# Kernel tuning notes

Measured on AMD Instinct MI355X. Metric: run time of the kernel, lower is better.

The kernel has to match this reference:

```python
import jax, jax.numpy as jnp
import numpy as np

# static config (matches init_kwargs)
B, H, W, C = 8, 64, 64, 512
HEADS, WS, SHIFT = 16, 8, 4
N = WS * WS
HIDDEN = 4 * C
HEAD_DIM = C // HEADS
SCALE = HEAD_DIM ** -0.5
EPS = 1e-3  # keras LayerNormalization default epsilon


def _rel_pos_index(ws):
    # replicates tf.meshgrid default 'xy' indexing used in the source
    coords = np.stack(np.meshgrid(np.arange(ws), np.arange(ws)))  # [2, ws, ws]
    cf = coords.reshape(2, -1)
    rel = (cf[:, :, None] - cf[:, None, :]).transpose(1, 2, 0)  # [N, N, 2]
    rel[:, :, 0] += ws - 1
    rel[:, :, 1] += ws - 1
    rel[:, :, 0] *= 2 * ws - 1
    return jnp.asarray(rel.sum(-1))  # [N, N] int


def _attn_mask(h, w, ws, shift):
    img = np.zeros((h, w), dtype=np.float32)
    cnt = 0
    for hs in (slice(0, -ws), slice(-ws, -shift), slice(-shift, None)):
        for wsl in (slice(0, -ws), slice(-ws, -shift), slice(-shift, None)):
            img[hs, wsl] = cnt
            cnt += 1
    mw = img.reshape(h // ws, ws, w // ws, ws).transpose(0, 2, 1, 3).reshape(-1, ws * ws)  # [nW, N]
    diff = mw[:, None, :] - mw[:, :, None]
    return jnp.asarray(np.where(diff != 0, -100.0, 0.0).astype(np.float32))  # [nW, N, N]


REL_IDX = _rel_pos_index(WS)
ATTN_MASK = _attn_mask(H, W, WS, SHIFT)
NW = (H // WS) * (W // WS)


def _ln(x, g, b):
    mu = jnp.mean(x, -1, keepdims=True)
    var = jnp.mean(jnp.square(x - mu), -1, keepdims=True)
    return (x - mu) * jax.lax.rsqrt(var + EPS) * g + b


def setup_inputs() -> dict:
    key = jax.random.key(0)
    ks = jax.random.split(key, 14)
    s = 0.02
    return {
        "x": jax.random.normal(ks[0], (B, H * W, C), jnp.float32),
        "norm1_g": jnp.ones((C,), jnp.float32),
        "norm1_b": jnp.zeros((C,), jnp.float32),
        "qkv_w": jax.random.normal(ks[1], (C, 3 * C), jnp.float32) * s,
        "qkv_b": jnp.zeros((3 * C,), jnp.float32),
        "rpb_table": jax.random.normal(ks[2], ((2 * WS - 1) ** 2, HEADS), jnp.float32) * s,
        "proj_w": jax.random.normal(ks[3], (C, C), jnp.float32) * s,
        "proj_b": jnp.zeros((C,), jnp.float32),
        "norm2_g": jnp.ones((C,), jnp.float32),
        "norm2_b": jnp.zeros((C,), jnp.float32),
        "fc1_w": jax.random.normal(ks[4], (C, HIDDEN), jnp.float32) * s,
        "fc1_b": jnp.zeros((HIDDEN,), jnp.float32),
        "fc2_w": jax.random.normal(ks[5], (HIDDEN, C), jnp.float32) * s,
        "fc2_b": jnp.zeros((C,), jnp.float32),
    }


def reference(x, norm1_g, norm1_b, qkv_w, qkv_b, rpb_table, proj_w, proj_b,
              norm2_g, norm2_b, fc1_w, fc1_b, fc2_w, fc2_b):
    shortcut = x
    h = _ln(x, norm1_g, norm1_b).reshape(B, H, W, C)
    # cyclic shift (SW-MSA)
    h = jnp.roll(h, (-SHIFT, -SHIFT), axis=(1, 2))
    # window partition -> (B*nW, N, C)
    h = h.reshape(B, H // WS, WS, W // WS, WS, C).transpose(0, 1, 3, 2, 4, 5)
    h = h.reshape(B * NW, N, C)
    # qkv
    qkv = (h @ qkv_w + qkv_b).reshape(B * NW, N, 3, HEADS, HEAD_DIM).transpose(2, 0, 3, 1, 4)
    q, k, v = qkv[0] * SCALE, qkv[1], qkv[2]  # each [Bw, heads, N, hd]
    attn = jnp.einsum('bhnd,bhmd->bhnm', q, k)  # [Bw, heads, N, N]
    bias = rpb_table[REL_IDX.reshape(-1)].reshape(N, N, HEADS).transpose(2, 0, 1)
    attn = attn + bias[None]
    # shifted-window mask, per source: mask add -> softmax -> softmax AGAIN (source quirk)
    attn = attn.reshape(B, NW, HEADS, N, N) + ATTN_MASK[None, :, None]
    attn = attn.reshape(B * NW, HEADS, N, N)
    attn = jax.nn.softmax(attn, axis=-1)
    attn = jax.nn.softmax(attn, axis=-1)
    o = jnp.einsum('bhnm,bhmd->bhnd', attn, v).transpose(0, 2, 1, 3).reshape(B * NW, N, C)
    o = o @ proj_w + proj_b
    # window reverse + reverse shift
    o = o.reshape(B, H // WS, W // WS, WS, WS, C).transpose(0, 1, 3, 2, 4, 5).reshape(B, H, W, C)
    o = jnp.roll(o, (SHIFT, SHIFT), axis=(1, 2)).reshape(B, H * W, C)
    x = shortcut + o
    # MLP: source applies gelu twice (Dense activation + explicit gelu)
    y = _ln(x, norm2_g, norm2_b)
    y = jax.nn.gelu(jax.nn.gelu(y @ fc1_w + fc1_b, approximate=False), approximate=False)
    y = y @ fc2_w + fc2_b
    return x + y
```

## Files before the change

### kernel.cpp

```cpp
#include <hip/hip_runtime.h>
#include <hip/hip_bf16.h>
#include <math.h>


typedef unsigned short ushort_t;
typedef __attribute__((ext_vector_type(8))) short short8;
typedef __attribute__((ext_vector_type(8))) __bf16 bf16x8;
typedef __attribute__((ext_vector_type(4))) float f32x4;

#define DEVINL __device__ __forceinline__

union frag_u { short8 s; bf16x8 b; };

DEVINL float bf2f(ushort_t u){ union {unsigned int i; float f;} c; c.i = ((unsigned)u)<<16; return c.f; }
DEVINL ushort_t f2bf(float f){ union {unsigned int i; float f;} c; c.f = f; unsigned r = c.i + 0x7fffu + ((c.i>>16)&1u); return (ushort_t)(r>>16); }

typedef const __attribute__((address_space(1))) void* gas_t;
typedef __attribute__((address_space(3))) void* las_t;
DEVINL void load_lds16(const void* g, void* l) {
  __builtin_amdgcn_global_load_lds((gas_t)g, (las_t)l, 16, 0, 0);
}

DEVINL float gelu_fast(float v){
  float z  = fabsf(v) * 0.70710678118654752f;
  float t  = __builtin_amdgcn_rcpf(fmaf(0.47047f, z, 1.0f));
  float p  = t * fmaf(t, fmaf(t, 0.7478556f, -0.0958798f), 0.3480242f);
  float e  = __expf(-z*z);
  float er = fmaf(-p, e, 1.0f);
  float hs = (v >= 0.f) ? 0.5f : -0.5f;
  return v * fmaf(hs, er, 0.5f);
}

DEVINL int win_map_row(int t){
  int bw = t >> 6, n = t & 63;
  int b  = bw >> 6, wdx = bw & 63;
  int wh = wdx >> 3, ww = wdx & 7;
  int r  = n >> 3,  c  = n & 7;
  int hh = (wh*8 + r + 4) & 63;
  int w2 = (ww*8 + c + 4) & 63;
  return (b << 12) + (hh << 6) + w2;
}

DEVINL void remap_mn(int bid, int nwg, int nbn, int BM, int BN, int& m0, int& n0){
  int q    = nwg >> 3;
  int lbid = (bid & 7)*q + (bid >> 3);
  m0 = (lbid / nbn) * BM;
  n0 = (lbid % nbn) * BN;
}

__global__ void transpose_all(const float* __restrict__ qkv_w, const float* __restrict__ proj_w,
                              const float* __restrict__ fc1_w, const float* __restrict__ fc2_w,
                              ushort_t* __restrict__ wqT, ushort_t* __restrict__ wpT,
                              ushort_t* __restrict__ w1T, ushort_t* __restrict__ w2T){
  __shared__ float t[32][33];
  int bid = blockIdx.x;
  const float* in; ushort_t* out; int R, Ccols, bx, by;
  if (bid < 768)      { in=qkv_w;  out=wqT; R=512;  Ccols=1536; bx=(bid%48)*32;        by=(bid/48)*32; }
  else if (bid < 1024){ int b=bid-768;  in=proj_w; out=wpT; R=512;  Ccols=512;  bx=(b%16)*32; by=(b/16)*32; }
  else if (bid < 2048){ int b=bid-1024; in=fc1_w;  out=w1T; R=512;  Ccols=2048; bx=(b%64)*32; by=(b/64)*32; }
  else                { int b=bid-2048; in=fc2_w;  out=w2T; R=2048; Ccols=512;  bx=(b%16)*32; by=(b/16)*32; }
  int x = threadIdx.x, y = threadIdx.y;
  #pragma unroll
  for (int i=0;i<32;i+=8) t[y+i][x] = in[(size_t)(by+y+i)*Ccols + bx + x];
  __syncthreads();
  #pragma unroll
  for (int i=0;i<32;i+=8) out[(size_t)(bx+y+i)*R + by + x] = f2bf(t[x][y+i]);
}

__global__ __launch_bounds__(256) void ln_kernel(const float* __restrict__ in,
    const float* __restrict__ g, const float* __restrict__ bta,
    ushort_t* __restrict__ out, int windowed){
  int tid = threadIdx.x; int l = tid & 63; int w = tid >> 6;
  int t = blockIdx.x * 4 + w;
  int src = windowed ? win_map_row(t) : t;
  const float* row = in + (size_t)src * 512;
  float4 v0 = *(const float4*)(row + l*8);
  float4 v1 = *(const float4*)(row + l*8 + 4);
  float f[8] = {v0.x,v0.y,v0.z,v0.w, v1.x,v1.y,v1.z,v1.w};
  float s=0.f, s2=0.f;
  #pragma unroll
  for (int j=0;j<8;j++){ s += f[j]; s2 += f[j]*f[j]; }
  #pragma unroll
  for (int m=1;m<64;m<<=1){ s += __shfl_xor(s,m); s2 += __shfl_xor(s2,m); }
  float mu  = s * (1.f/512.f);
  float var = s2*(1.f/512.f) - mu*mu;
  float rs  = rsqrtf(var + 1e-3f);
  float4 g0 = *(const float4*)(g + l*8),   g1 = *(const float4*)(g + l*8 + 4);
  float4 b0 = *(const float4*)(bta + l*8), b1 = *(const float4*)(bta + l*8 + 4);
  float gg[8] = {g0.x,g0.y,g0.z,g0.w, g1.x,g1.y,g1.z,g1.w};
  float bb[8] = {b0.x,b0.y,b0.z,b0.w, b1.x,b1.y,b1.z,b1.w};
  short8 o;
  #pragma unroll
  for (int j=0;j<8;j++) o[j] = (short)f2bf((f[j]-mu)*rs*gg[j] + bb[j]);
  *(short8*)(out + (size_t)t*512 + l*8) = o;
}

#define G_STAGE(G, base, h, tt, LB) do { \
    load_lds16((G) + (base) + (size_t)((h)*128)*K    + (size_t)(tt)*64, &lds[(LB) + (h)*8192 +        w*512]); \
    load_lds16((G) + (base) + (size_t)((h)*128+64)*K + (size_t)(tt)*64, &lds[(LB) + (h)*8192 + 4096 + w*512]); \
  } while(0)

#define NOWAIT
#define VM4 asm volatile("s_waitcnt vmcnt(4)" ::: "memory")

#define PHASE(mp, STAGE_STMT, EXTRA) do { \
    bf16x8 a0 = *(const bf16x8*)&lds[ALb + aoff[2*(mp)  ][0]]; \
    bf16x8 a1 = *(const bf16x8*)&lds[ALb + aoff[2*(mp)  ][1]]; \
    bf16x8 a2 = *(const bf16x8*)&lds[ALb + aoff[2*(mp)+1][0]]; \
    bf16x8 a3 = *(const bf16x8*)&lds[ALb + aoff[2*(mp)+1][1]]; \
    STAGE_STMT; \
    EXTRA; \
    __builtin_amdgcn_s_barrier(); \
    asm volatile("s_waitcnt lgkmcnt(0)" ::: "memory"); \
    __builtin_amdgcn_sched_barrier(0); \
    __builtin_amdgcn_s_setprio(1); \
    _Pragma("unroll") \
    for (int nf=0; nf<4; nf++){ \
      acc[2*(mp)  ][nf] = __builtin_amdgcn_mfma_f32_16x16x32_bf16(a0, bfr[nf][0], acc[2*(mp)  ][nf], 0,0,0); \
      acc[2*(mp)  ][nf] = __builtin_amdgcn_mfma_f32_16x16x32_bf16(a1, bfr[nf][1], acc[2*(mp)  ][nf], 0,0,0); \
      acc[2*(mp)+1][nf] = __builtin_amdgcn_mfma_f32_16x16x32_bf16(a2, bfr[nf][0], acc[2*(mp)+1][nf], 0,0,0); \
      acc[2*(mp)+1][nf] = __builtin_amdgcn_mfma_f32_16x16x32_bf16(a3, bfr[nf][1], acc[2*(mp)+1][nf], 0,0,0); \
    } \
    __builtin_amdgcn_s_setprio(0); \
    __builtin_amdgcn_sched_barrier(0); \
    __builtin_amdgcn_s_barrier(); \
  } while(0)

template<int EPI>
__global__ __launch_bounds__(512, 2) void gemm256(
    const ushort_t* __restrict__ A, const ushort_t* __restrict__ Bt,
    const float* __restrict__ bias, void* __restrict__ Cout_v,
    const float* __restrict__ xres, int M, int N, int K, int nbn)
{
  __shared__ ushort_t lds[65536];
  const int tid = threadIdx.x; const int l = tid & 63; const int w = tid >> 6;
  const int wm = w >> 2, wn = w & 3;
  int m0, n0;
  remap_mn(blockIdx.x, gridDim.x, nbn, 256, 256, m0, n0);
  const int lr = l & 15, lk = l >> 4;
  const int nt = K >> 6;

  const int r0 = tid >> 3;
  const int kc = ((tid & 7) - r0) & 7;
  const size_t aRow0 = (size_t)(m0 + r0) * K + kc * 8;
  const size_t bRow0 = (size_t)(n0 + r0) * K + kc * 8;

  int aoff[8][2], boff[4][2];
  #pragma unroll
  for (int mf=0; mf<8; mf++){
    int row = wm*128 + mf*16 + lr;
    #pragma unroll
    for (int kh=0; kh<2; kh++){ int c = kh*4 + lk; aoff[mf][kh] = (row*8 + ((c + row)&7))*8; }
  }
  #pragma unroll
  for (int nf=0; nf<4; nf++){
    int row = wn*64 + nf*16 + lr;
    #pragma unroll
    for (int kh=0; kh<2; kh++){ int c = kh*4 + lk; boff[nf][kh] = (row*8 + ((c + row)&7))*8; }
  }

  f32x4 acc[8][4] = {};

  G_STAGE(A,  aRow0, 0, 0, 0);
  G_STAGE(A,  aRow0, 1, 0, 0);
  G_STAGE(Bt, bRow0, 0, 0, 16384);
  G_STAGE(Bt, bRow0, 1, 0, 16384);
  G_STAGE(Bt, bRow0, 0, 1, 32768+16384);
  G_STAGE(Bt, bRow0, 1, 1, 32768+16384);
  VM4;
  __builtin_amdgcn_s_barrier();

  for (int t = 0; t < nt; ++t) {
    const int b   = t & 1;
    const int ALb = b*32768, BLb = ALb + 16384;
    const int ALn = (b^1)*32768;
    const int t1  = (t+1 < nt) ? t+1 : t;
    const int t2  = (t+2 < nt) ? t+2 : t;

    bf16x8 bfr[4][2];
    #pragma unroll
    for (int nf=0; nf<4; nf++){
      bfr[nf][0] = *(const bf16x8*)&lds[BLb + boff[nf][0]];
      bfr[nf][1] = *(const bf16x8*)&lds[BLb + boff[nf][1]];
    }
    PHASE(0, G_STAGE(A,  aRow0, 0, t1, ALn), NOWAIT);
    PHASE(1, G_STAGE(A,  aRow0, 1, t1, ALn), NOWAIT);
    PHASE(2, G_STAGE(Bt, bRow0, 0, t2, BLb), NOWAIT);
    PHASE(3, G_STAGE(Bt, bRow0, 1, t2, BLb), VM4);
  }

  asm volatile("s_waitcnt vmcnt(0)" ::: "memory");
  __builtin_amdgcn_s_barrier();

  int erow = l >> 2, ecc = l & 3;
  if (EPI == 0){
    ushort_t* tw = lds + w*1152;
    #pragma unroll
    for (int mf=0; mf<8; mf++){
      #pragma unroll
      for (int nf=0; nf<4; nf++){
        float bz = bias[n0 + wn*64 + nf*16 + lr];
        #pragma unroll
        for (int rg=0; rg<4; rg++)
          tw[(lk*4+rg)*72 + nf*16 + lr] = f2bf(acc[mf][nf][rg] + bz);
      }
      short8 p0 = *(const short8*)(tw + erow*72 + ecc*16);
      short8 p1 = *(const short8*)(tw + erow*72 + ecc*16 + 8);
      int grow = m0 + wm*128 + mf*16 + erow;
      int col  = n0 + wn*64 + ecc*16;
      *(short8*)&((ushort_t*)Cout_v)[(size_t)grow*N + col]     = p0;
      *(short8*)&((ushort_t*)Cout_v)[(size_t)grow*N + col + 8] = p1;
    }
  } else {
    float* twf = (float*)lds + w*1152;
    #pragma unroll
    for (int mf=0; mf<8; mf++){
      #pragma unroll
      for (int nf=0; nf<4; nf++){
        float bz = bias[n0 + wn*64 + nf*16 + lr];
        #pragma unroll
        for (int rg=0; rg<4; rg++)
          twf[(lk*4+rg)*72 + nf*16 + lr] = acc[mf][nf][rg] + bz;
      }
      int grow = m0 + wm*128 + mf*16 + erow;
      int col  = n0 + wn*64 + ecc*16;
      float4 q0 = *(const float4*)(twf + erow*72 + ecc*16);
      float4 q1 = *(const float4*)(twf + erow*72 + ecc*16 + 4);
      float4 q2 = *(const float4*)(twf + erow*72 + ecc*16 + 8);
      float4 q3 = *(const float4*)(twf + erow*72 + ecc*16 + 12);
      size_t off;
      if (EPI == 2){
        int row2 = win_map_row(grow);
        off = (size_t)row2*512 + col;
        float4 x0 = *(const float4*)(xres + off);
        float4 x1 = *(const float4*)(xres + off + 4);
        float4 x2 = *(const float4*)(xres + off + 8);
        float4 x3 = *(const float4*)(xres + off + 12);
        q0 = make_float4(q0.x+x0.x, q0.y+x0.y, q0.z+x0.z, q0.w+x0.w);
        q1 = make_float4(q1.x+x1.x, q1.y+x1.y, q1.z+x1.z, q1.w+x1.w);
        q2 = make_float4(q2.x+x2.x, q2.y+x2.y, q2.z+x2.z, q2.w+x2.w);
        q3 = make_float4(q3.x+x3.x, q3.y+x3.y, q3.z+x3.z, q3.w+x3.w);
      } else {
        off = (size_t)grow*N + col;
        float* o = (float*)Cout_v;
        float4 x0 = *(const float4*)(o + off);
        float4 x1 = *(const float4*)(o + off + 4);
        float4 x2 = *(const float4*)(o + off + 8);
        float4 x3 = *(const float4*)(o + off + 12);
        q0 = make_float4(q0.x+x0.x, q0.y+x0.y, q0.z+x0.z, q0.w+x0.w);
        q1 = make_float4(q1.x+x1.x, q1.y+x1.y, q1.z+x1.z, q1.w+x1.w);
        q2 = make_float4(q2.x+x2.x, q2.y+x2.y, q2.z+x2.z, q2.w+x2.w);
        q3 = make_float4(q3.x+x3.x, q3.y+x3.y, q3.z+x3.z, q3.w+x3.w);
      }
      float* o = (float*)Cout_v;
      *(float4*)(o + off)      = q0;
      *(float4*)(o + off + 4)  = q1;
      *(float4*)(o + off + 8)  = q2;
      *(float4*)(o + off + 12) = q3;
    }
  }
}

template<int EPI>
__global__ __launch_bounds__(512, 4) void gemmv(
    const ushort_t* __restrict__ A, const ushort_t* __restrict__ Bt,
    const float* __restrict__ bias, void* __restrict__ Cout_v,
    const float* __restrict__ xres, int M, int N, int K, int nbn)
{
  __shared__ ushort_t lds[24576];
  __shared__ float g2tab[(EPI==1)?2048:1];
  const int tid = threadIdx.x; const int l = tid & 63; const int w = tid >> 6;
  const int wm = w >> 1, wn = w & 1;
  int m0, n0; remap_mn(blockIdx.x, gridDim.x, nbn, 256, 128, m0, n0);
  const int lr = l & 15, lk = l >> 4;
  const int nt = K >> 5;

  if (EPI == 1){
    #pragma unroll
    for (int i=0;i<4;i++){
      int idx = tid*4 + i;
      float vi = -4.f + (float)idx*(1.f/256.f);
      g2tab[idx] = gelu_fast(gelu_fast(vi));
    }
  }

  const int r0 = tid >> 2;
  const int kc = ((tid & 3) - (r0 >> 1)) & 3;
  const size_t aG = (size_t)(m0 + r0) * K + kc*8;
  const size_t bG = (size_t)(n0 + r0) * K + kc*8;

  #define STAGE_T(tt, LB) do { \
    load_lds16(A  + aG +                  (size_t)(tt)*32, &lds[(LB) +        w*512]); \
    load_lds16(A  + aG + 128*(size_t)K +  (size_t)(tt)*32, &lds[(LB) + 4096 + w*512]); \
    load_lds16(Bt + bG +                  (size_t)(tt)*32, &lds[(LB) + 8192 + w*512]); \
  } while(0)

  int aoff[4], boff[4];
  #pragma unroll
  for (int mf=0; mf<4; mf++){
    int row = wm*64 + mf*16 + lr;
    aoff[mf] = (row*4 + ((lk + (row>>1)) & 3))*8;
  }
  #pragma unroll
  for (int nf=0; nf<4; nf++){
    int row = wn*64 + nf*16 + lr;
    boff[nf] = 8192 + (row*4 + ((lk + (row>>1)) & 3))*8;
  }

  f32x4 acc[4][4] = {};

  STAGE_T(0, 0);
  STAGE_T(1, 12288);
  asm volatile("s_waitcnt vmcnt(3)" ::: "memory");
  __builtin_amdgcn_s_barrier();

  for (int t = 0; t < nt; ++t){
    const int Lb = (t & 1) ? 12288 : 0;
    const int t2 = (t+2 < nt) ? t+2 : nt-1;
    bf16x8 af[4], bfr[4];
    #pragma unroll
    for (int mf=0; mf<4; mf++) af[mf]  = *(const bf16x8*)&lds[Lb + aoff[mf]];
    #pragma unroll
    for (int nf=0; nf<4; nf++) bfr[nf] = *(const bf16x8*)&lds[Lb + boff[nf]];
    __builtin_amdgcn_sched_barrier(0);
    asm volatile("s_waitcnt lgkmcnt(0)" ::: "memory");
    __builtin_amdgcn_s_barrier();
    __builtin_amdgcn_sched_barrier(0);
    STAGE_T(t2, Lb);
    __builtin_amdgcn_sched_barrier(0);
    __builtin_amdgcn_s_setprio(1);
    #pragma unroll
    for (int mf=0; mf<4; mf++)
      #pragma unroll
      for (int nf=0; nf<4; nf++)
        acc[mf][nf] = __builtin_amdgcn_mfma_f32_16x16x32_bf16(af[mf], bfr[nf], acc[mf][nf], 0,0,0);
    __builtin_amdgcn_s_setprio(0);
    __builtin_amdgcn_sched_barrier(0);
    asm volatile("s_waitcnt vmcnt(3)" ::: "memory");
    __builtin_amdgcn_s_barrier();
  }

  asm volatile("s_waitcnt vmcnt(0)" ::: "memory");
  __builtin_amdgcn_s_barrier();
  __builtin_amdgcn_sched_barrier(0);

  int erow = l >> 2, ecc = l & 3;
  ushort_t* tw = lds + w*1152;
  #pragma unroll
  for (int mf=0; mf<4; mf++){
    #pragma unroll
    for (int nf=0; nf<4; nf++){
      float bz = bias[n0 + wn*64 + nf*16 + lr];
      #pragma unroll
      for (int rg=0; rg<4; rg++){
        float v = acc[mf][nf][rg] + bz;
        if (EPI == 1){
          float u  = fminf(fmaxf(fmaf(v, 256.f, 1024.5f), 0.f), 2047.f);
          float rr = g2tab[(int)u];
          rr = (v >  4.f) ? v   : rr;
          v  = (v < -4.f) ? 0.f : rr;
        }
        tw[(lk*4+rg)*72 + nf*16 + lr] = f2bf(v);
      }
    }
    short8 p0 = *(const short8*)(tw + erow*72 + ecc*16);
    short8 p1 = *(const short8*)(tw + erow*72 + ecc*16 + 8);
    int grow = m0 + wm*64 + mf*16 + erow;
    int col  = n0 + wn*64 + ecc*16;
    *(short8*)&((ushort_t*)Cout_v)[(size_t)grow*N + col]     = p0;
    *(short8*)&((ushort_t*)Cout_v)[(size_t)grow*N + col + 8] = p1;
  }
  #undef STAGE_T
}

DEVINL int band3(int t){ return (t<56) ? 0 : ((t<60) ? 1 : 2); }

__global__ __launch_bounds__(256) void attn_kernel(const ushort_t* __restrict__ qkv,
    const float* __restrict__ rpb, ushort_t* __restrict__ o)
{
  __shared__ ushort_t sP[4][64*64];
  __shared__ ushort_t sV[4][64*32];
  int tid = threadIdx.x; int l = tid & 63; int w = tid >> 6;
  int p = blockIdx.x*4 + w;
  int bw = p >> 4, head = p & 15;
  int lr = l & 15, lk = l >> 4;
  const ushort_t* base = qkv + (size_t)bw*64*1536 + head*32;

  #pragma unroll
  for (int c=0;c<4;c++){
    int idx = c*64 + l;
    int row = idx >> 2, cc = idx & 3;
    load_lds16(base + 1024 + (size_t)row*1536 + cc*8, &sV[w][0] + c*512);
  }

  bf16x8 qf[4], kf[4];
  #pragma unroll
  for (int m=0;m<4;m++) qf[m] = *(const bf16x8*)(base +       (size_t)(m*16+lr)*1536 + lk*8);
  #pragma unroll
  for (int m=0;m<4;m++) kf[m] = *(const bf16x8*)(base + 512 + (size_t)(m*16+lr)*1536 + lk*8);

  f32x4 s[4][4] = {};
  #pragma unroll
  for (int m=0;m<4;m++)
    #pragma unroll
    for (int n=0;n<4;n++)
      s[m][n] = __builtin_amdgcn_mfma_f32_16x16x32_bf16(qf[m], kf[n], s[m][n], 0,0,0);

  int wdx = bw & 63; int wh = wdx >> 3, ww = wdx & 7;
  const float SCALE = 0.17677669529663687f;
  #pragma unroll
  for (int m=0;m<4;m++){
    #pragma unroll
    for (int r=0;r<4;r++){
      int i  = m*16 + lk*4 + r;
      int ri = band3(wh*8 + (i>>3))*3 + band3(ww*8 + (i&7));
      int ix = i & 7, iy = i >> 3;
      #pragma unroll
      for (int n=0;n<4;n++){
        int j   = n*16 + lr;
        int rj  = band3(wh*8 + (j>>3))*3 + band3(ww*8 + (j&7));
        int idx = 15*(ix - (j&7) + 7) + (iy - (j>>3) + 7);
        float bv = rpb[idx*16 + head];
        float mk = (ri == rj) ? 0.f : -100.f;
        s[m][n][r] = s[m][n][r]*SCALE + bv + mk;
      }
    }
  }

  #pragma unroll
  for (int pass=0; pass<2; pass++){
    #pragma unroll
    for (int m=0;m<4;m++){
      #pragma unroll
      for (int r=0;r<4;r++){
        float mx = fmaxf(fmaxf(s[m][0][r], s[m][1][r]), fmaxf(s[m][2][r], s[m][3][r]));
        #pragma unroll
        for (int d=1;d<16;d<<=1) mx = fmaxf(mx, __shfl_xor(mx, d));
        float sum = 0.f;
        #pragma unroll
        for (int n=0;n<4;n++){ float e = __expf(s[m][n][r]-mx); s[m][n][r]=e; sum += e; }
        #pragma unroll
        for (int d=1;d<16;d<<=1) sum += __shfl_xor(sum, d);
        float inv = 1.f/sum;
        #pragma unroll
        for (int n=0;n<4;n++) s[m][n][r] = s[m][n][r]*inv;
      }
    }
  }

  ushort_t* pl = &sP[w][0];
  #pragma unroll
  for (int m=0;m<4;m++)
    #pragma unroll
    for (int r=0;r<4;r++){
      int i = m*16 + lk*4 + r;
      #pragma unroll
      for (int n=0;n<4;n++){
        int j = n*16 + lr;
        int byte = i*128 + ((j*2) ^ ((i&7)<<4));
        pl[byte>>1] = f2bf(s[m][n][r]);
      }
    }

  asm volatile("s_waitcnt vmcnt(0)" ::: "memory");
  const ushort_t* vl = &sV[w][0];
  frag_u vf[2][2];
  #pragma unroll
  for (int kb=0;kb<2;kb++)
    #pragma unroll
    for (int nb=0;nb<2;nb++){
      #pragma unroll
      for (int j=0;j<8;j++){
        int k = kb*32 + lk*8 + j;
        vf[kb][nb].s[j] = (short)vl[k*32 + nb*16 + lr];
      }
    }

  f32x4 oacc[4][2] = {};
  #pragma unroll
  for (int m=0;m<4;m++){
    #pragma unroll
    for (int kb=0;kb<2;kb++){
      int row  = m*16 + lr;
      int byte = row*128 + ((kb*64 + lk*16) ^ ((row&7)<<4));
      bf16x8 pf = *(const bf16x8*)(pl + (byte>>1));
      #pragma unroll
      for (int nb=0;nb<2;nb++)
        oacc[m][nb] = __builtin_amdgcn_mfma_f32_16x16x32_bf16(pf, vf[kb][nb].b, oacc[m][nb], 0,0,0);
    }
  }

  ushort_t* orow = o + (size_t)bw*64*512 + head*32;
  #pragma unroll
  for (int m=0;m<4;m++)
    #pragma unroll
    for (int nb=0;nb<2;nb++)
      #pragma unroll
      for (int r=0;r<4;r++){
        int i = m*16 + lk*4 + r;
        int d = nb*16 + lr;
        orow[(size_t)i*512 + d] = f2bf(oacc[m][nb][r]);
      }
}

extern "C" void kernel_launch(void* const* d_in, const int* in_sizes, int n_in,
                              void* d_out, int out_size, void* d_ws, size_t ws_size,
                              hipStream_t stream) {
  const float* x      = (const float*)d_in[0];
  const float* n1g    = (const float*)d_in[1];
  const float* n1b    = (const float*)d_in[2];
  const float* qkv_w  = (const float*)d_in[3];
  const float* qkv_b  = (const float*)d_in[4];
  const float* rpb    = (const float*)d_in[5];
  const float* proj_w = (const float*)d_in[6];
  const float* proj_b = (const float*)d_in[7];
  const float* n2g    = (const float*)d_in[8];
  const float* n2b    = (const float*)d_in[9];
  const float* fc1_w  = (const float*)d_in[10];
  const float* fc1_b  = (const float*)d_in[11];
  const float* fc2_w  = (const float*)d_in[12];
  const float* fc2_b  = (const float*)d_in[13];
  float* out = (float*)d_out;

  ushort_t* ws = (ushort_t*)d_ws;
  size_t off = 0;
  ushort_t* wqT = ws + off; off += (size_t)1536*512;
  ushort_t* wpT = ws + off; off += (size_t)512*512;
  ushort_t* w1T = ws + off; off += (size_t)2048*512;
  ushort_t* w2T = ws + off; off += (size_t)512*2048;
  ushort_t* R1  = ws + off; off += (size_t)32768*512;
  ushort_t* R2  = ws + off; off += (size_t)32768*2048;
  if (ws_size < off*sizeof(ushort_t)) return;

  transpose_all<<<3072, dim3(32,8), 0, stream>>>(qkv_w, proj_w, fc1_w, fc2_w, wqT, wpT, w1T, w2T);

  ln_kernel<<<8192, 256, 0, stream>>>(x, n1g, n1b, R1, 1);
  gemm256<0><<<768, 512, 0, stream>>>(R1, wqT, qkv_b, R2, nullptr, 32768, 1536, 512, 6);
  attn_kernel<<<2048, 256, 0, stream>>>(R2, rpb, R1);
  gemm256<2><<<256, 512, 0, stream>>>(R1, wpT, proj_b, out, x, 32768, 512, 512, 2);
  ln_kernel<<<8192, 256, 0, stream>>>(out, n2g, n2b, R1, 0);
  gemmv<1><<<2048, 512, 0, stream>>>(R1, w1T, fc1_b, R2, nullptr, 32768, 2048, 512, 16);
  gemm256<3><<<256, 512, 0, stream>>>(R2, w2T, fc2_b, out, nullptr, 32768, 512, 2048, 2);
}
```

Before: 389.5 us.

## Triple-buffer gemm K loop and route fc2 through smaller-tile kernel

The 256x128 tiled GEMM grows from double to triple LDS buffering, prefetching three K-steps ahead so more global loads are in flight. To fit the larger LDS footprint, the GELU lookup table is halved to 1024 entries at coarser resolution. A new fp32 accumulate-into-output epilogue lets the fc2 GEMM use this kernel, giving 512 blocks instead of 256 with the larger 256x256 kernel and so better occupancy across CUs. The trade-offs are more LDS per block, which may reduce resident blocks, and a coarser GELU approximation.

```diff
diff --git a/kernel.cpp b/kernel.cpp
--- a/kernel.cpp
+++ b/kernel.cpp
@@ -229,6 +229,7 @@
       float4 q2 = *(const float4*)(twf + erow*72 + ecc*16 + 8);
       float4 q3 = *(const float4*)(twf + erow*72 + ecc*16 + 12);
       size_t off;
+      float* o = (float*)Cout_v;
       if (EPI == 2){
         int row2 = win_map_row(grow);
         off = (size_t)row2*512 + col;
@@ -242,7 +243,6 @@
         q3 = make_float4(q3.x+x3.x, q3.y+x3.y, q3.z+x3.z, q3.w+x3.w);
       } else {
         off = (size_t)grow*N + col;
-        float* o = (float*)Cout_v;
         float4 x0 = *(const float4*)(o + off);
         float4 x1 = *(const float4*)(o + off + 4);
         float4 x2 = *(const float4*)(o + off + 8);
@@ -252,7 +252,6 @@
         q2 = make_float4(q2.x+x2.x, q2.y+x2.y, q2.z+x2.z, q2.w+x2.w);
         q3 = make_float4(q3.x+x3.x, q3.y+x3.y, q3.z+x3.z, q3.w+x3.w);
       }
-      float* o = (float*)Cout_v;
       *(float4*)(o + off)      = q0;
       *(float4*)(o + off + 4)  = q1;
       *(float4*)(o + off + 8)  = q2;
@@ -262,13 +261,13 @@
 }
 
 template<int EPI>
-__global__ __launch_bounds__(512, 4) void gemmv(
+__global__ __launch_bounds__(512, 4) void gemmw(
     const ushort_t* __restrict__ A, const ushort_t* __restrict__ Bt,
     const float* __restrict__ bias, void* __restrict__ Cout_v,
     const float* __restrict__ xres, int M, int N, int K, int nbn)
 {
-  __shared__ ushort_t lds[24576];
-  __shared__ float g2tab[(EPI==1)?2048:1];
+  __shared__ ushort_t lds[36864];
+  __shared__ float g2tab[(EPI==1)?1024:1];
   const int tid = threadIdx.x; const int l = tid & 63; const int w = tid >> 6;
   const int wm = w >> 1, wn = w & 1;
   int m0, n0; remap_mn(blockIdx.x, gridDim.x, nbn, 256, 128, m0, n0);
@@ -277,9 +276,9 @@
 
   if (EPI == 1){
     #pragma unroll
-    for (int i=0;i<4;i++){
-      int idx = tid*4 + i;
-      float vi = -4.f + (float)idx*(1.f/256.f);
+    for (int i=0;i<2;i++){
+      int idx = tid*2 + i;
+      float vi = -4.f + (float)idx*(1.f/128.f);
       g2tab[idx] = gelu_fast(gelu_fast(vi));
     }
   }
@@ -311,12 +310,13 @@
 
   STAGE_T(0, 0);
   STAGE_T(1, 12288);
-  asm volatile("s_waitcnt vmcnt(3)" ::: "memory");
+  STAGE_T(2, 24576);
+  asm volatile("s_waitcnt vmcnt(6)" ::: "memory");
   __builtin_amdgcn_s_barrier();
 
+  int Lb = 0;
   for (int t = 0; t < nt; ++t){
-    const int Lb = (t & 1) ? 12288 : 0;
-    const int t2 = (t+2 < nt) ? t+2 : nt-1;
+    const int t3 = (t+3 < nt) ? t+3 : nt-1;
     bf16x8 af[4], bfr[4];
     #pragma unroll
     for (int mf=0; mf<4; mf++) af[mf]  = *(const bf16x8*)&lds[Lb + aoff[mf]];
@@ -326,7 +326,7 @@
     asm volatile("s_waitcnt lgkmcnt(0)" ::: "memory");
     __builtin_amdgcn_s_barrier();
     __builtin_amdgcn_sched_barrier(0);
-    STAGE_T(t2, Lb);
+    STAGE_T(t3, Lb);
     __builtin_amdgcn_sched_barrier(0);
     __builtin_amdgcn_s_setprio(1);
     #pragma unroll
@@ -336,8 +336,9 @@
         acc[mf][nf] = __builtin_amdgcn_mfma_f32_16x16x32_bf16(af[mf], bfr[nf], acc[mf][nf], 0,0,0);
     __builtin_amdgcn_s_setprio(0);
     __builtin_amdgcn_sched_barrier(0);
-    asm volatile("s_waitcnt vmcnt(3)" ::: "memory");
+    asm volatile("s_waitcnt vmcnt(6)" ::: "memory");
     __builtin_amdgcn_s_barrier();
+    Lb += 12288; if (Lb == 36864) Lb = 0;
   }
 
   asm volatile("s_waitcnt vmcnt(0)" ::: "memory");
@@ -345,30 +346,62 @@
   __builtin_amdgcn_sched_barrier(0);
 
   int erow = l >> 2, ecc = l & 3;
-  ushort_t* tw = lds + w*1152;
-  #pragma unroll
-  for (int mf=0; mf<4; mf++){
-    #pragma unroll
-    for (int nf=0; nf<4; nf++){
-      float bz = bias[n0 + wn*64 + nf*16 + lr];
-      #pragma unroll
-      for (int rg=0; rg<4; rg++){
-        float v = acc[mf][nf][rg] + bz;
-        if (EPI == 1){
-          float u  = fminf(fmaxf(fmaf(v, 256.f, 1024.5f), 0.f), 2047.f);
+  if (EPI == 1){
+    ushort_t* tw = lds + w*1152;
+    #pragma unroll
+    for (int mf=0; mf<4; mf++){
+      #pragma unroll
+      for (int nf=0; nf<4; nf++){
+        float bz = bias[n0 + wn*64 + nf*16 + lr];
+        #pragma unroll
+        for (int rg=0; rg<4; rg++){
+          float v = acc[mf][nf][rg] + bz;
+          float u  = fminf(fmaxf(fmaf(v, 128.f, 512.5f), 0.f), 1023.f);
           float rr = g2tab[(int)u];
           rr = (v >  4.f) ? v   : rr;
           v  = (v < -4.f) ? 0.f : rr;
+          tw[(lk*4+rg)*72 + nf*16 + lr] = f2bf(v);
         }
-        tw[(lk*4+rg)*72 + nf*16 + lr] = f2bf(v);
-      }
-    }
-    short8 p0 = *(const short8*)(tw + erow*72 + ecc*16);
-    short8 p1 = *(const short8*)(tw + erow*72 + ecc*16 + 8);
-    int grow = m0 + wm*64 + mf*16 + erow;
-    int col  = n0 + wn*64 + ecc*16;
-    *(short8*)&((ushort_t*)Cout_v)[(size_t)grow*N + col]     = p0;
-    *(short8*)&((ushort_t*)Cout_v)[(size_t)grow*N + col + 8] = p1;
+      }
+      short8 p0 = *(const short8*)(tw + erow*72 + ecc*16);
+      short8 p1 = *(const short8*)(tw + erow*72 + ecc*16 + 8);
+      int grow = m0 + wm*64 + mf*16 + erow;
+      int col  = n0 + wn*64 + ecc*16;
+      *(short8*)&((ushort_t*)Cout_v)[(size_t)grow*N + col]     = p0;
+      *(short8*)&((ushort_t*)Cout_v)[(size_t)grow*N + col + 8] = p1;
+    }
+  } else {
+    float* twf = (float*)lds + w*1152;
+    #pragma unroll
+    for (int mf=0; mf<4; mf++){
+      #pragma unroll
+      for (int nf=0; nf<4; nf++){
+        float bz = bias[n0 + wn*64 + nf*16 + lr];
+        #pragma unroll
+        for (int rg=0; rg<4; rg++)
+          twf[(lk*4+rg)*72 + nf*16 + lr] = acc[mf][nf][rg] + bz;
+      }
+      int grow = m0 + wm*64 + mf*16 + erow;
+      int col  = n0 + wn*64 + ecc*16;
+      float4 q0 = *(const float4*)(twf + erow*72 + ecc*16);
+      float4 q1 = *(const float4*)(twf + erow*72 + ecc*16 + 4);
+      float4 q2 = *(const float4*)(twf + erow*72 + ecc*16 + 8);
+      float4 q3 = *(const float4*)(twf + erow*72 + ecc*16 + 12);
+      float* o = (float*)Cout_v;
+      size_t off = (size_t)grow*N + col;
+      float4 x0 = *(const float4*)(o + off);
+      float4 x1 = *(const float4*)(o + off + 4);
+      float4 x2 = *(const float4*)(o + off + 8);
+      float4 x3 = *(const float4*)(o + off + 12);
+      q0 = make_float4(q0.x+x0.x, q0.y+x0.y, q0.z+x0.z, q0.w+x0.w);
+      q1 = make_float4(q1.x+x1.x, q1.y+x1.y, q1.z+x1.z, q1.w+x1.w);
+      q2 = make_float4(q2.x+x2.x, q2.y+x2.y, q2.z+x2.z, q2.w+x2.w);
+      q3 = make_float4(q3.x+x3.x, q3.y+x3.y, q3.z+x3.z, q3.w+x3.w);
+      *(float4*)(o + off)      = q0;
+      *(float4*)(o + off + 4)  = q1;
+      *(float4*)(o + off + 8)  = q2;
+      *(float4*)(o + off + 12) = q3;
+    }
   }
   #undef STAGE_T
 }
@@ -539,6 +572,6 @@
   attn_kernel<<<2048, 256, 0, stream>>>(R2, rpb, R1);
   gemm256<2><<<256, 512, 0, stream>>>(R1, wpT, proj_b, out, x, 32768, 512, 512, 2);
   ln_kernel<<<8192, 256, 0, stream>>>(out, n2g, n2b, R1, 0);
-  gemmv<1><<<2048, 512, 0, stream>>>(R1, w1T, fc1_b, R2, nullptr, 32768, 2048, 512, 16);
-  gemm256<3><<<256, 512, 0, stream>>>(R2, w2T, fc2_b, out, nullptr, 32768, 512, 2048, 2);
-}
+  gemmw<1><<<2048, 512, 0, stream>>>(R1, w1T, fc1_b, R2, nullptr, 32768, 2048, 512, 16);
+  gemmw<3><<<512, 512, 0, stream>>>(R2, w2T, fc2_b, out, nullptr, 32768, 512, 2048, 4);
+}
```

Measured after the change: 404.8 us. 3.9% more time.

## Split-K the fc2 GEMM with atomic accumulation into the residual output

Applied to the files above, without the earlier changes.

Replaces the 256-block fc2 GEMM (K=2048) with a new split-K kernel that uses 2048 blocks of 128x128-ish tiles over four K slices of 512. Each slice atomically adds its partial sums, plus the bias on the first slice, into the output buffer that already holds the residual. This is meant to fix the low block count of the old launch, which left much of the GPU idle. In exchange it adds float atomic traffic to a 32768x512 fp32 output and makes the summation order nondeterministic.

```diff
diff --git a/kernel.cpp b/kernel.cpp
--- a/kernel.cpp
+++ b/kernel.cpp
@@ -229,6 +229,7 @@
       float4 q2 = *(const float4*)(twf + erow*72 + ecc*16 + 8);
       float4 q3 = *(const float4*)(twf + erow*72 + ecc*16 + 12);
       size_t off;
+      float* o = (float*)Cout_v;
       if (EPI == 2){
         int row2 = win_map_row(grow);
         off = (size_t)row2*512 + col;
@@ -242,7 +243,6 @@
         q3 = make_float4(q3.x+x3.x, q3.y+x3.y, q3.z+x3.z, q3.w+x3.w);
       } else {
         off = (size_t)grow*N + col;
-        float* o = (float*)Cout_v;
         float4 x0 = *(const float4*)(o + off);
         float4 x1 = *(const float4*)(o + off + 4);
         float4 x2 = *(const float4*)(o + off + 8);
@@ -252,7 +252,6 @@
         q2 = make_float4(q2.x+x2.x, q2.y+x2.y, q2.z+x2.z, q2.w+x2.w);
         q3 = make_float4(q3.x+x3.x, q3.y+x3.y, q3.z+x3.z, q3.w+x3.w);
       }
-      float* o = (float*)Cout_v;
       *(float4*)(o + off)      = q0;
       *(float4*)(o + off + 4)  = q1;
       *(float4*)(o + off + 8)  = q2;
@@ -369,6 +368,95 @@
     int col  = n0 + wn*64 + ecc*16;
     *(short8*)&((ushort_t*)Cout_v)[(size_t)grow*N + col]     = p0;
     *(short8*)&((ushort_t*)Cout_v)[(size_t)grow*N + col + 8] = p1;
+  }
+  #undef STAGE_T
+}
+
+__global__ __launch_bounds__(512, 4) void gemmsk(
+    const ushort_t* __restrict__ A, const ushort_t* __restrict__ Bt,
+    const float* __restrict__ bias, float* __restrict__ Cout, int M, int N, int K)
+{
+  __shared__ ushort_t lds[24576];
+  const int tid = threadIdx.x; const int l = tid & 63; const int w = tid >> 6;
+  const int wm = w >> 1, wn = w & 1;
+  const int nwg = gridDim.x;
+  int q    = nwg >> 3;
+  int lbid = ((blockIdx.x & 7)*q + (blockIdx.x >> 3));
+  const int ksl  = lbid >> 9;
+  const int tile = lbid & 511;
+  const int m0 = (tile >> 2) * 256;
+  const int n0 = (tile & 3) * 128;
+  const int lr = l & 15, lk = l >> 4;
+  const int nt = 16;
+
+  const int r0 = tid >> 2;
+  const int kc = ((tid & 3) - (r0 >> 1)) & 3;
+  const size_t aG = (size_t)(m0 + r0) * K + (size_t)ksl*512 + kc*8;
+  const size_t bG = (size_t)(n0 + r0) * K + (size_t)ksl*512 + kc*8;
+
+  #define STAGE_T(tt, LB) do { \
+    load_lds16(A  + aG +                  (size_t)(tt)*32, &lds[(LB) +        w*512]); \
+    load_lds16(A  + aG + 128*(size_t)K +  (size_t)(tt)*32, &lds[(LB) + 4096 + w*512]); \
+    load_lds16(Bt + bG +                  (size_t)(tt)*32, &lds[(LB) + 8192 + w*512]); \
+  } while(0)
+
+  int aoff[4], boff[4];
+  #pragma unroll
+  for (int mf=0; mf<4; mf++){
+    int row = wm*64 + mf*16 + lr;
+    aoff[mf] = (row*4 + ((lk + (row>>1)) & 3))*8;
+  }
+  #pragma unroll
+  for (int nf=0; nf<4; nf++){
+    int row = wn*64 + nf*16 + lr;
+    boff[nf] = 8192 + (row*4 + ((lk + (row>>1)) & 3))*8;
+  }
+
+  f32x4 acc[4][4] = {};
+
+  STAGE_T(0, 0);
+  STAGE_T(1, 12288);
+  asm volatile("s_waitcnt vmcnt(3)" ::: "memory");
+  __builtin_amdgcn_s_barrier();
+
+  for (int t = 0; t < nt; ++t){
+    const int Lb = (t & 1) ? 12288 : 0;
+    const int t2 = (t+2 < nt) ? t+2 : nt-1;
+    bf16x8 af[4], bfr[4];
+    #pragma unroll
+    for (int mf=0; mf<4; mf++) af[mf]  = *(const bf16x8*)&lds[Lb + aoff[mf]];
+    #pragma unroll
+    for (int nf=0; nf<4; nf++) bfr[nf] = *(const bf16x8*)&lds[Lb + boff[nf]];
+    __builtin_amdgcn_sched_barrier(0);
+    asm volatile("s_waitcnt lgkmcnt(0)" ::: "memory");
+    __builtin_amdgcn_s_barrier();
+    __builtin_amdgcn_sched_barrier(0);
+    STAGE_T(t2, Lb);
+    __builtin_amdgcn_sched_barrier(0);
+    __builtin_amdgcn_s_setprio(1);
+    #pragma unroll
+    for (int mf=0; mf<4; mf++)
+      #pragma unroll
+      for (int nf=0; nf<4; nf++)
+        acc[mf][nf] = __builtin_amdgcn_mfma_f32_16x16x32_bf16(af[mf], bfr[nf], acc[mf][nf], 0,0,0);
+    __builtin_amdgcn_s_setprio(0);
+    __builtin_amdgcn_sched_barrier(0);
+    asm volatile("s_waitcnt vmcnt(3)" ::: "memory");
+    __builtin_amdgcn_s_barrier();
+  }
+
+  #pragma unroll
+  for (int mf=0; mf<4; mf++){
+    int rbase = m0 + wm*64 + mf*16 + lk*4;
+    #pragma unroll
+    for (int nf=0; nf<4; nf++){
+      int col = n0 + wn*64 + nf*16 + lr;
+      float bz = (ksl == 0) ? bias[col] : 0.f;
+      #pragma unroll
+      for (int rg=0; rg<4; rg++){
+        atomicAdd(&Cout[(size_t)(rbase+rg)*N + col], acc[mf][nf][rg] + bz);
+      }
+    }
   }
   #undef STAGE_T
 }
@@ -540,5 +628,5 @@
   gemm256<2><<<256, 512, 0, stream>>>(R1, wpT, proj_b, out, x, 32768, 512, 512, 2);
   ln_kernel<<<8192, 256, 0, stream>>>(out, n2g, n2b, R1, 0);
   gemmv<1><<<2048, 512, 0, stream>>>(R1, w1T, fc1_b, R2, nullptr, 32768, 2048, 512, 16);
-  gemm256<3><<<256, 512, 0, stream>>>(R2, w2T, fc2_b, out, nullptr, 32768, 512, 2048, 2);
-}
+  gemmsk<<<2048, 512, 0, stream>>>(R2, w2T, fc2_b, out, 32768, 512, 2048);
+}
```

New measurement: 536.2 us. 1.38x slower.
